# Kernel optimization log

Measured on AMD Instinct MI355X. Metric: run time of the kernel, lower is better.

## Reference

```python
import jax, jax.numpy as jnp
import numpy as np

KSIZE, STRIDE, RATE, FUSE_K, SCALE = 3, 1, 2, 3, 10.0
ESCAPE_NAN = 1e-4


def same_pad(x, k, s):
    # torch same_padding: pad so out = ceil(in/s)
    H, W = x.shape[2], x.shape[3]
    oh, ow = -(-H // s), -(-W // s)
    ph = max(0, (oh - 1) * s + k - H)
    pw = max(0, (ow - 1) * s + k - W)
    return jnp.pad(x, ((0, 0), (0, 0), (ph // 2, ph - ph // 2), (pw // 2, pw - pw // 2)))


def extract_patches(x, k, s):
    # torch Unfold -> view(B,C,k,k,L) -> permute(0,4,1,2,3): returns [B, L, C, k, k]
    x = same_pad(x, k, s)
    B, C, H, W = x.shape
    oh, ow = (H - k) // s + 1, (W - k) // s + 1
    rows = jnp.arange(oh)[:, None] * s + jnp.arange(k)[None, :]
    cols = jnp.arange(ow)[:, None] * s + jnp.arange(k)[None, :]
    p = x[:, :, rows][:, :, :, :, cols]  # [B,C,oh,k,ow,k]
    return p.transpose(0, 2, 4, 1, 3, 5).reshape(B, oh * ow, C, k, k)


def conv1x1(x, w, b):
    return jnp.einsum('bchw,oc->bohw', x, w) + b[None, :, None, None]


def conv2d(x, w):
    return jax.lax.conv_general_dilated(x, w, (1, 1), 'VALID',
                                        dimension_numbers=('NCHW', 'OIHW', 'NCHW'))


def conv_transpose2d(x, w, stride, pad):
    # matches F.conv_transpose2d(x, w[Cin,Cout,k,k], stride, padding=pad)
    k = w.shape[2]
    wf = jnp.flip(w, (2, 3))
    return jax.lax.conv_general_dilated(x, wf, (1, 1), [(k - 1 - pad, k - 1 - pad)] * 2,
                                        lhs_dilation=(stride, stride),
                                        dimension_numbers=('NCHW', 'IOHW', 'NCHW'))


def global_attention(a, bm, c, wq, bq, wk, bk, wv, bv, gamma):
    # a,bm: [B,C,H,W]; c: [B,1,Hc,Wc]; mask scales score rows before softmax
    B, C, H, W = a.shape
    dr = c.shape[2] // H
    c = c[:, :, ::dr, ::dr]  # nearest downsample, matches F.interpolate(mode='nearest')
    q = conv1x1(a, wq, bq).reshape(B, C, H * W)
    k = conv1x1(bm, wk, bk).reshape(B, C, H * W)
    sim = jnp.einsum('bci,bcj->bij', q, k)  # [B,N,N]
    mv = c.reshape(B, H * W)
    attn = jax.nn.softmax(sim * mv[:, :, None], axis=-1)
    v = conv1x1(a, wv, bv).reshape(B, C, H * W)
    out = jnp.einsum('bcj,bij->bci', v, attn).reshape(B, C, H, W)
    return gamma * a * c + (1.0 - c) * out


def _forward(f, b, mask, fa, pa):
    B, C, H, W = b.shape
    kernel = 2 * RATE
    raw_w = extract_patches(b, kernel, RATE * STRIDE)  # [B, L, C, 4, 4]
    f_ds = f[:, :, ::RATE, ::RATE]
    b_ds = b[:, :, ::RATE, ::RATE]
    Hd, Wd = f_ds.shape[2], f_ds.shape[3]
    mask0 = mask[0:1]  # torch uses m_groups[0] for all samples
    dr = mask0.shape[2] // Hd
    mask_ds = mask0[:, :, ::dr, ::dr]  # [1,1,Hd,Wd]
    w = extract_patches(b_ds, KSIZE, STRIDE)   # [B, L, C, 3, 3]
    fw = extract_patches(f_ds, KSIZE, STRIDE)  # [B, L, C, 3, 3]
    m = extract_patches(mask_ds, KSIZE, STRIDE)[0]  # [L, 1, 3, 3]
    mm = (jnp.mean(m, axis=(1, 2, 3), keepdims=True) == 0.0).astype(f.dtype)
    mm = mm.transpose(1, 0, 2, 3)  # [1, L, 1, 1]
    fuse_w = jnp.eye(FUSE_K, dtype=f.dtype).reshape(1, 1, FUSE_K, FUSE_K)

    def per_sample(xi, bi, fi_p, wi_p, raw_wi):
        # patch-level attention refines the dynamic conv kernels
        fp_p = global_attention(fi_p, wi_p, m, *pa)  # [L, C, 3, 3]
        norm = jnp.sqrt(jnp.sum(fp_p * fp_p, axis=(1, 2, 3), keepdims=True))
        wi_n = fp_p / jnp.maximum(norm, ESCAPE_NAN)
        # feature-level attention on the downsampled foreground
        fp = global_attention(xi[None], bi[None], mask_ds, *fa)  # [1,C,Hd,Wd]
        yi = conv2d(same_pad(fp, KSIZE, 1), wi_n)  # [1, L, Hd, Wd]
        Nb = Hd * Wd
        # fuse: identity-kernel smoothing over (bg-pos, fg-pos) score plane, twice
        yi = yi.reshape(1, 1, Nb, Nb)
        yi = conv2d(same_pad(yi, FUSE_K, 1), fuse_w)
        yi = yi.reshape(1, Hd, Wd, Hd, Wd).transpose(0, 2, 1, 4, 3).reshape(1, 1, Nb, Nb)
        yi = conv2d(same_pad(yi, FUSE_K, 1), fuse_w)
        yi = yi.reshape(1, Wd, Hd, Wd, Hd).transpose(0, 2, 1, 4, 3)
        yi = yi.reshape(1, Nb, Hd, Wd)
        yi = jax.nn.softmax(yi * mm * SCALE, axis=1) * mm
        return conv_transpose2d(yi, raw_wi, RATE, 1)[0] / 4.0  # [C, H, W]

    return jax.vmap(per_sample)(f_ds, b_ds, fw, w, raw_w)


def setup_inputs() -> dict:
    key = jax.random.key(0)
    ks = jax.random.split(key, 10)
    B, C, H, W = 2, 64, 96, 96
    f = jax.random.normal(ks[0], (B, C, H, W), jnp.float32)
    b = jax.random.normal(ks[1], (B, C, H, W), jnp.float32)
    mask = (jax.random.uniform(ks[2], (B, 1, H, W)) < 0.25).astype(jnp.float32)

    def wmat(k):
        return jax.random.normal(k, (C, C), jnp.float32) * 0.05

    return {
        'f': f, 'b': b, 'mask': mask,
        'fa_wq': wmat(ks[3]), 'fa_bq': jnp.zeros((C,), jnp.float32),
        'fa_wk': wmat(ks[4]), 'fa_bk': jnp.zeros((C,), jnp.float32),
        'fa_wv': wmat(ks[5]), 'fa_bv': jnp.zeros((C,), jnp.float32),
        'fa_gamma': jnp.ones((1,), jnp.float32),
        'pa_wq': wmat(ks[6]), 'pa_bq': jnp.zeros((C,), jnp.float32),
        'pa_wk': wmat(ks[7]), 'pa_bk': jnp.zeros((C,), jnp.float32),
        'pa_wv': wmat(ks[8]), 'pa_bv': jnp.zeros((C,), jnp.float32),
        'pa_gamma': jnp.ones((1,), jnp.float32),
    }


def reference(f, b, mask, fa_wq, fa_bq, fa_wk, fa_bk, fa_wv, fa_bv, fa_gamma,
              pa_wq, pa_bq, pa_wk, pa_bk, pa_wv, pa_bv, pa_gamma):
    fa = (fa_wq, fa_bq, fa_wk, fa_bk, fa_wv, fa_bv, fa_gamma)
    pa = (pa_wq, pa_bq, pa_wk, pa_bk, pa_wv, pa_bv, pa_gamma)
    return _forward(f, b, mask, fa, pa)
```

## Files before the change

### kernel.cpp

```cpp
#include <hip/hip_runtime.h>
#include <math.h>

#define HD 48
#define NB 2304
#define NC 64
#define IMG 96
#define NP 2401
#define KP 2432

#define CDIV(a,b) (((a)+(b)-1)/(b))

typedef unsigned short u16;
typedef __attribute__((ext_vector_type(8))) short  s16x8;
typedef __attribute__((ext_vector_type(8))) unsigned short u16x8;
typedef __attribute__((ext_vector_type(4))) float  f32x4;

constexpr size_t O_MASKDS = 0;
constexpr size_t O_MMP    = NB;
constexpr size_t O_CMAX   = (size_t)2*NB;
constexpr size_t O_CINV   = (size_t)4*NB;
constexpr size_t O_PMAX   = (size_t)6*NB;
constexpr size_t O_PSUM   = (size_t)38*NB;
constexpr size_t O_MEAN   = (size_t)70*NB;
constexpr size_t O_ACT    = (size_t)70*NB + 256;
constexpr size_t O_ROWIDX = O_ACT + 2434/1 + 62;
constexpr size_t O_INVROW = O_ROWIDX + 2560;
constexpr size_t O_NROW   = O_INVROW + NB;
constexpr size_t O_NEEDX  = O_NROW + 64;
constexpr size_t O_ZPAD   = O_NEEDX + NB;
constexpr size_t O_ARENA0 = O_NEEDX + NB + 64;
constexpr size_t A_FDS  = 0;
constexpr size_t A_FDST = 147456;
constexpr size_t A_SCR  = 294912;
constexpr size_t A_P0   = A_SCR + 2654208;
constexpr size_t A_P1   = A_P0 + (size_t)NB*NB;
constexpr size_t A_Y    = A_P1 + 5839232;
constexpr size_t A_B4   = A_Y + (size_t)NB*NB;
constexpr size_t SSTR   = A_B4 + 622592;
constexpr size_t TOTAL_F = O_ARENA0 + 2*SSTR;

__device__ inline void split_bf16(float x, u16& hi, u16& lo){
  unsigned int u = __float_as_uint(x);
  unsigned int r = u + 0x7FFFu + ((u >> 16) & 1u);
  hi = (u16)(r >> 16);
  float xh = __uint_as_float(((unsigned int)hi) << 16);
  float res = x - xh;
  unsigned int u2 = __float_as_uint(res);
  unsigned int r2 = u2 + 0x7FFFu + ((u2 >> 16) & 1u);
  lo = (u16)(r2 >> 16);
}

__device__ __forceinline__ void gload16(const u16* g, u16* l){
  __builtin_amdgcn_global_load_lds(
      (const __attribute__((address_space(1))) unsigned int*)g,
      (__attribute__((address_space(3))) unsigned int*)l, 16, 0, 0);
}


__global__ void k_prep(const float* __restrict__ mask, float* __restrict__ maskds,
                       float* __restrict__ mmP,
                       int* __restrict__ actIdx, int* __restrict__ nActPad,
                       int* __restrict__ rowIdx, int* __restrict__ invRow,
                       int* __restrict__ nRowPad, float* __restrict__ needXf,
                       u16* __restrict__ zp){
  __shared__ float lmm[NB];
  __shared__ unsigned char needX[NB], needS[NB];
  __shared__ int cnt[256], base[256];
  int tid = threadIdx.x;
  for(int q=tid; q<NB; q+=256){
    int hq = q/HD, wq = q%HD;
    maskds[q] = mask[(2*hq)*IMG + 2*wq];
    float any = 0.f;
    for(int u=-1;u<=1;u++)
      for(int v=-1;v<=1;v++){
        int y=hq+u, x=wq+v;
        if(y>=0&&y<HD&&x>=0&&x<HD) any += mask[(2*y)*IMG + 2*x];
      }
    float v = (any == 0.f) ? 1.f : 0.f;
    mmP[wq*HD + hq] = v;
    lmm[wq*HD + hq] = v;
  }
  if(tid < 16) ((unsigned int*)zp)[tid] = 0u;
  __syncthreads();
  {
    int c0 = tid*10, c1 = min(c0+10, NP);
    int flags = 0, lc = 0;
    for(int i=c0;i<c1;i++){
      int ph=i/49, pw=i%49;
      bool act=false;
      #pragma unroll
      for(int a=0;a<2;a++)
        #pragma unroll
        for(int bb=0;bb<2;bb++){
          int sh=ph-a, sw=pw-bb;
          if(sh>=0&&sh<HD&&sw>=0&&sw<HD && lmm[sw*HD+sh]!=0.f) act=true;
        }
      if(act){ flags |= 1<<(i-c0); lc++; }
    }
    cnt[tid]=lc;
    __syncthreads();
    if(tid==0){
      int run=0;
      for(int i=0;i<256;i++){ base[i]=run; run+=cnt[i]; }
      int pad=(run+63)&~63;
      nActPad[0]=pad; nActPad[1]=run;
      for(int k=run;k<pad;k++) actIdx[k]=NP;
    }
    __syncthreads();
    int o=base[tid];
    for(int i=c0;i<c1;i++) if(flags & (1<<(i-c0))) actIdx[o++]=i;
  }
  __syncthreads();
  {
    for(int i=tid;i<NB;i+=256) needX[i]=0;
    __syncthreads();
    for(int qp=tid; qp<NB; qp+=256){
      if(lmm[qp]!=0.f){
        #pragma unroll
        for(int d=-1;d<=1;d++){
          int rb=qp+d; if(rb<0||rb>=NB) continue;
          int b2=rb/HD, a=rb%HD;
          needX[a*HD + b2] = 1;
        }
      }
    }
    __syncthreads();
    for(int r=tid;r<NB;r+=256){
      unsigned char v = needX[r];
      if(r>0)    v |= needX[r-1];
      if(r<NB-1) v |= needX[r+1];
      needS[r]=v;
    }
    __syncthreads();
    int c0 = tid*9, c1 = min(c0+9, NB);
    int lc=0; for(int i=c0;i<c1;i++) lc += needS[i];
    cnt[tid]=lc;
    __syncthreads();
    if(tid==0){
      int run=0;
      for(int i=0;i<256;i++){ base[i]=run; run+=cnt[i]; }
      int pad=(run+127)&~127;
      nRowPad[0]=pad; nRowPad[1]=run;
      for(int k=run;k<pad;k++) rowIdx[k]=NB;
    }
    __syncthreads();
    int o=base[tid];
    for(int i=c0;i<c1;i++){
      if(needS[i]){ rowIdx[o]=i; invRow[i]=o; o++; }
      else invRow[i] = -1;
    }
    for(int i=tid;i<NB;i+=256) needXf[i] = needX[i] ? 1.f : 0.f;
  }
}

__global__ void k_ds(const float* __restrict__ src, float* __restrict__ fds0,
                     float* __restrict__ fdsT0){
  int s = blockIdx.y;
  float* fds  = fds0  + (size_t)s*SSTR;
  float* fdsT = fdsT0 + (size_t)s*SSTR;
  int idx = blockIdx.x*256 + threadIdx.x;
  if(idx >= NC*NB) return;
  int c = idx/NB, j = idx%NB;
  int h = j/HD, w = j%HD;
  float v = src[(((size_t)s*NC + c)*IMG + 2*h)*IMG + 2*w];
  fds[idx] = v;
  fdsT[(size_t)j*64 + c] = v;
}

__global__ void k_colmean(const float* __restrict__ fds0, float* __restrict__ meanf){
  int s = blockIdx.y;
  const float* fds = fds0 + (size_t)s*SSTR;
  int c = blockIdx.x;
  int tid = threadIdx.x;
  float sum = 0.f;
  for(int j=tid; j<NB; j+=256) sum += fds[(size_t)c*NB + j];
  for(int off=32; off>0; off>>=1) sum += __shfl_down(sum, off);
  __shared__ float red[4];
  if((tid&63)==0) red[tid>>6] = sum;
  __syncthreads();
  if(tid==0) meanf[s*64 + c] = (red[0]+red[1]+red[2]+red[3]) * (1.f/NB);
}

__global__ void k_meanvf(const float* __restrict__ meanf, const float* __restrict__ wv,
                         const float* __restrict__ bv, float* __restrict__ meanVf){
  int s = blockIdx.x;
  __shared__ float mf[64];
  int c = threadIdx.x;
  mf[c] = meanf[s*64 + c];
  __syncthreads();
  float sum = 0.f;
  for(int cc=0;cc<64;cc++) sum += wv[c*64+cc]*mf[cc];
  meanVf[s*64 + c] = sum + bv[c];
}

__global__ void k_stageA(const float* __restrict__ fdsT0, const float* __restrict__ maskds,
                         const float* __restrict__ wv, const float* __restrict__ bv,
                         const float* __restrict__ gammap,
                         u16* __restrict__ AH0, u16* __restrict__ AL0){
  int s = blockIdx.y;
  const float* fdsT = fdsT0 + (size_t)s*SSTR;
  u16* AH = AH0 + (size_t)s*2*SSTR;
  u16* AL = AL0 + (size_t)s*2*SSTR;
  __shared__ float sumA[4][64];
  __shared__ float mval[4][9];
  int wsl = threadIdx.x>>6;
  int c = threadIdx.x&63;
  int p = blockIdx.x*4 + wsl;
  int ph = p/HD, pw = p%HD;
  float A[9]; float sa = 0.f;
  #pragma unroll
  for(int i=0;i<9;i++){
    int u=i/3, v=i%3;
    int y=ph+u-1, x=pw+v-1;
    bool in = (y>=0&&y<HD&&x>=0&&x<HD);
    float fv = in ? fdsT[(size_t)(y*HD+x)*64 + c] : 0.f;
    A[i] = fv; sa += fv;
    if(c==0) mval[wsl][i] = in ? maskds[y*HD+x] : 0.f;
  }
  sumA[wsl][c] = sa;
  __syncthreads();
  float acc = 0.f;
  for(int cc=0;cc<64;cc++) acc += wv[c*64+cc]*sumA[wsl][cc];
  float meanVc = acc*(1.f/9.f) + bv[c];
  float gamma = gammap[0];
  float fpv[9]; float ss = 0.f;
  #pragma unroll
  for(int i=0;i<9;i++){
    float v = (mval[wsl][i]!=0.f) ? gamma*A[i] : meanVc;
    fpv[i] = v; ss += v*v;
  }
  for(int off=32; off>0; off>>=1) ss += __shfl_down(ss, off);
  ss = __shfl(ss, 0);
  float scale = 1.f / fmaxf(sqrtf(ss), 1e-4f);
  #pragma unroll
  for(int i=0;i<9;i++){
    u16 h,l; split_bf16(fpv[i]*scale, h, l);
    size_t o = (size_t)p*576 + c*9 + i;
    AH[o] = h; AL[o] = l;
  }
}

__global__ void k_bcolT_split(const float* __restrict__ fds0, const float* __restrict__ maskds,
                              const float* __restrict__ meanVf, const float* __restrict__ gfp,
                              u16* __restrict__ BTH0, u16* __restrict__ BTL0){
  int s = blockIdx.y;
  const float* fds = fds0 + (size_t)s*SSTR;
  u16* BTH = BTH0 + (size_t)s*2*SSTR;
  u16* BTL = BTL0 + (size_t)s*2*SSTR;
  int idx = blockIdx.x*256 + threadIdx.x;
  if(idx >= NB*576) return;
  int P = idx/576, k = idx%576;
  int c = k/9, i = k%9, u = i/3, v = i%3;
  int hP = P/HD, wP = P%HD;
  int y = hP+u-1, x = wP+v-1;
  float val = 0.f;
  if(y>=0&&y<HD&&x>=0&&x<HD){
    int pos = y*HD + x;
    val = (maskds[pos]!=0.f) ? gfp[0]*fds[(size_t)c*NB + pos] : meanVf[s*64 + c];
  }
  u16 h,l; split_bf16(val, h, l);
  BTH[idx] = h; BTL[idx] = l;
}

__global__ __launch_bounds__(256, 2)
void k_gemm4(const u16* __restrict__ AH0, const u16* __restrict__ AL0,
             const u16* __restrict__ BTH0, const u16* __restrict__ BTL0,
             float* __restrict__ C0, int M, int N, int Kparam, int nz,
             const int* __restrict__ Kdev,
             const int* __restrict__ rowIdx, const int* __restrict__ Mdev,
             const u16* __restrict__ zp,
             int ldA, int ldB, int ldC, long zstrC){
  __shared__ u16 sAH[2][128*32], sAL[2][128*32], sBH[2][128*32], sBL[2][128*32];
  int tid = threadIdx.x;
  int s = blockIdx.z / nz, zk = blockIdx.z % nz;
  int Mout = Mdev ? Mdev[0] : M;
  int gx = gridDim.x;
  int nwg = gx*gridDim.y;
  int orig = blockIdx.y*gx + blockIdx.x;
  int xcd = orig & 7;
  int qq = nwg>>3, rr2 = nwg&7;
  int swz = (xcd<rr2 ? xcd*(qq+1) : rr2*(qq+1) + (xcd-rr2)*qq) + (orig>>3);
  int by = swz/gx, bx = swz - by*gx;
  int m0 = by*128, n0 = bx*128;
  if(m0 >= Mout) return;
  const u16* AH  = AH0  + (size_t)s*2*SSTR;
  const u16* AL  = AL0  + (size_t)s*2*SSTR;
  const u16* BTH = BTH0 + (size_t)s*2*SSTR;
  const u16* BTL = BTL0 + (size_t)s*2*SSTR;
  float* Cz = C0 + (size_t)s*SSTR + (size_t)zk*zstrC;
  int K = Kdev ? Kdev[0] : Kparam;
  int Kc = (((K+31)/32 + nz - 1)/nz)*32;
  int kbeg = zk*Kc; int kend = kbeg+Kc; if(kend>K) kend=K;
  int w = tid>>6, lane = tid&63;
  int wr = w>>1, wc = w&1;
  int fr = lane&15, fq = lane>>4;

  int ch0 = w, ch1 = 4+w;
  int rl0 = ch0*16 + (lane>>2), rl1 = ch1*16 + (lane>>2);
  int gp = lane&3;
  int gr0 = (gp ^ ((rl0>>1)&3))*8;
  int gr1 = (gp ^ ((rl1>>1)&3))*8;
  int mi0 = m0+rl0, mi1 = m0+rl1;
  int ar0 = rowIdx ? rowIdx[mi0] : mi0;
  int ar1 = rowIdx ? rowIdx[mi1] : mi1;
  bool av0 = (ar0 < M), av1 = (ar1 < M);
  int br0 = n0+rl0, br1 = n0+rl1;
  bool bv0 = (br0 < N), bv1 = (br1 < N);
  const u16* pAH0 = AH + (size_t)(av0?ar0:0)*ldA + gr0;
  const u16* pAH1 = AH + (size_t)(av1?ar1:0)*ldA + gr1;
  const u16* pAL0 = AL + (size_t)(av0?ar0:0)*ldA + gr0;
  const u16* pAL1 = AL + (size_t)(av1?ar1:0)*ldA + gr1;
  const u16* pBH0 = BTH + (size_t)(bv0?br0:0)*ldB + gr0;
  const u16* pBH1 = BTH + (size_t)(bv1?br1:0)*ldB + gr1;
  const u16* pBL0 = BTL + (size_t)(bv0?br0:0)*ldB + gr0;
  const u16* pBL1 = BTL + (size_t)(bv1?br1:0)*ldB + gr1;
  int lo0 = ch0*512, lo1 = ch1*512;

#define GISSUE(BUF, K0) { \
    gload16(av0 ? pAH0+(K0) : zp, &sAH[BUF][lo0]); \
    gload16(av1 ? pAH1+(K0) : zp, &sAH[BUF][lo1]); \
    gload16(av0 ? pAL0+(K0) : zp, &sAL[BUF][lo0]); \
    gload16(av1 ? pAL1+(K0) : zp, &sAL[BUF][lo1]); \
    gload16(bv0 ? pBH0+(K0) : zp, &sBH[BUF][lo0]); \
    gload16(bv1 ? pBH1+(K0) : zp, &sBH[BUF][lo1]); \
    gload16(bv0 ? pBL0+(K0) : zp, &sBL[BUF][lo0]); \
    gload16(bv1 ? pBL1+(K0) : zp, &sBL[BUF][lo1]); }

  f32x4 acc[4][4];
  #pragma unroll
  for(int i=0;i<4;i++)
    #pragma unroll
    for(int j=0;j<4;j++) acc[i][j] = (f32x4){0.f,0.f,0.f,0.f};

  if(kbeg < kend){ GISSUE(0, kbeg); }
  __syncthreads();
  int cur = 0;
  for(int k0=kbeg; k0<kend; k0+=32){
    if(k0+32 < kend) GISSUE(cur^1, k0+32);
    s16x8 a_h[4],a_l[4],b_h[4],b_l[4];
    #pragma unroll
    for(int mi=0;mi<4;mi++){
      int row=wr*64+mi*16+fr; int gs=(fq^((row>>1)&3))*8;
      a_h[mi]=*(const s16x8*)&sAH[cur][row*32+gs];
      a_l[mi]=*(const s16x8*)&sAL[cur][row*32+gs];
    }
    #pragma unroll
    for(int ni=0;ni<4;ni++){
      int row=wc*64+ni*16+fr; int gs=(fq^((row>>1)&3))*8;
      b_h[ni]=*(const s16x8*)&sBH[cur][row*32+gs];
      b_l[ni]=*(const s16x8*)&sBL[cur][row*32+gs];
    }
    #pragma unroll
    for(int mi=0;mi<4;mi++)
      #pragma unroll
      for(int ni=0;ni<4;ni++){
        acc[mi][ni] = __builtin_amdgcn_mfma_f32_16x16x32_bf16(a_h[mi], b_h[ni], acc[mi][ni], 0,0,0);
        acc[mi][ni] = __builtin_amdgcn_mfma_f32_16x16x32_bf16(a_h[mi], b_l[ni], acc[mi][ni], 0,0,0);
        acc[mi][ni] = __builtin_amdgcn_mfma_f32_16x16x32_bf16(a_l[mi], b_h[ni], acc[mi][ni], 0,0,0);
      }
    __syncthreads();
    cur ^= 1;
  }
#undef GISSUE
  #pragma unroll
  for(int mi=0;mi<4;mi++)
    #pragma unroll
    for(int ni=0;ni<4;ni++){
      int row = m0 + wr*64 + mi*16 + fq*4;
      int col = n0 + wc*64 + ni*16 + fr;
      if(col < N){
        #pragma unroll
        for(int rr=0;rr<4;rr++)
          if(row+rr < Mout) Cz[(size_t)(row+rr)*ldC + col] = acc[mi][ni][rr];
      }
    }
}

__global__ void k_fuseP(const float* __restrict__ Sb, const int* __restrict__ invRow,
                        const float* __restrict__ needXf, float* __restrict__ Yb){
  int s = blockIdx.y;
  int r = blockIdx.x;
  if(needXf[r] == 0.f) return;
  const float* S = Sb + (size_t)s*SSTR;
  float* Y = Yb + (size_t)s*SSTR;
  int i0 = invRow[r];
  int im = (r>0)    ? invRow[r-1] : -1;
  int ip = (r<NB-1) ? invRow[r+1] : -1;
  __shared__ float lds[48*49];
  const float* row0 = S + (size_t)i0*NB;
  for(int t=threadIdx.x; t<NB; t+=256){
    float v = row0[t];
    if(im>=0 && t>0)    v += S[(size_t)im*NB + t-1];
    if(ip>=0 && t<NB-1) v += S[(size_t)ip*NB + t+1];
    lds[(t/HD)*49 + (t%HD)] = v;
  }
  __syncthreads();
  int a = r/HD, b2 = r%HD;
  float* orow = Y + (size_t)(b2*HD + a)*NB;
  for(int t=threadIdx.x; t<NB; t+=256){
    int d = t/HD, c = t%HD;
    orow[t] = lds[c*49 + d];
  }
}

__global__ void k_fuse_colsm(const float* __restrict__ Yb, const float* __restrict__ mmP,
                             float* __restrict__ pmax, float* __restrict__ psum){
  int s = blockIdx.z;
  const float* Y = Yb + (size_t)s*SSTR;
  int col = blockIdx.x*256 + threadIdx.x;
  int q0 = blockIdx.y*144;
  float mx = -1e30f, sum = 0.f;
  for(int q=q0; q<q0+144; q++){
    if(mmP[q] == 0.f) continue;
    float L = Y[(size_t)q*NB + col];
    if(q>0 && col>0)       L += Y[(size_t)(q-1)*NB + col-1];
    if(q<NB-1 && col<NB-1) L += Y[(size_t)(q+1)*NB + col+1];
    L *= 10.f;
    if(L > mx){ sum *= __expf(mx - L); mx = L; }
    sum += __expf(L - mx);
  }
  pmax[(size_t)(s*16 + blockIdx.y)*NB + col] = mx;
  psum[(size_t)(s*16 + blockIdx.y)*NB + col] = sum;
}

__global__ void k_combine(const float* __restrict__ pmax, const float* __restrict__ psum,
                          const float* __restrict__ mmP,
                          float* __restrict__ cmax, float* __restrict__ cinv){
  int s = blockIdx.y;
  int col = blockIdx.x*256 + threadIdx.x;
  int tid = threadIdx.x;
  __shared__ float redc[4];
  float cnt = 0.f;
  for(int k=tid; k<NB; k+=256) cnt += mmP[k];
  for(int off=32; off>0; off>>=1) cnt += __shfl_down(cnt, off);
  if((tid&63)==0) redc[tid>>6] = cnt;
  __syncthreads();
  float nAct = redc[0]+redc[1]+redc[2]+redc[3];
  float M = -1e30f;
  for(int k=0;k<16;k++) M = fmaxf(M, pmax[(size_t)(s*16+k)*NB + col]);
  if(nAct < NB - 0.5f) M = fmaxf(M, 0.f);
  float S = 0.f;
  for(int k=0;k<16;k++){
    float pm = pmax[(size_t)(s*16+k)*NB + col];
    float ps = psum[(size_t)(s*16+k)*NB + col];
    S += ps * __expf(pm - M);
  }
  S += ((float)NB - nAct) * __expf(0.f - M);
  cmax[s*NB + col] = M;
  cinv[s*NB + col] = 1.f/S;
}

__global__ void k_fuse_apply(const float* __restrict__ Yb, const float* __restrict__ mmP,
                             const float* __restrict__ cmax, const float* __restrict__ cinv,
                             float* __restrict__ yiTb){
  int s = blockIdx.y;
  const float* Y = Yb + (size_t)s*SSTR;
  float* yiT = yiTb + (size_t)s*SSTR;
  const float* cm = cmax + s*NB;
  const float* ci = cinv + s*NB;
  __shared__ float lds[48*49];
  int alpha = blockIdx.x/HD, delta = blockIdx.x%HD;
  for(int t=threadIdx.x; t<NB; t+=256){
    int beta = t/HD, gamma = t%HD;
    int qp = beta*HD + alpha;
    int Pp = delta*HD + gamma;
    float v = 0.f;
    if(mmP[qp] != 0.f){
      float L = Y[(size_t)qp*NB + Pp];
      if(qp>0 && Pp>0)       L += Y[(size_t)(qp-1)*NB + Pp-1];
      if(qp<NB-1 && Pp<NB-1) L += Y[(size_t)(qp+1)*NB + Pp+1];
      v = __expf(10.f*L - cm[Pp]) * ci[Pp];
    }
    lds[beta*49 + gamma] = v;
  }
  __syncthreads();
  for(int t=threadIdx.x; t<NB; t+=256){
    int gamma = t/HD, beta = t%HD;
    if(mmP[beta*HD + alpha] != 0.f)
      yiT[(size_t)(gamma*HD + delta)*NB + alpha*HD + beta] = lds[beta*49 + gamma];
  }
}

__global__ void k_zbuildT_split(const float* __restrict__ yiTb, const float* __restrict__ mmP,
                                const int* __restrict__ actIdx, const int* __restrict__ nActPad,
                                u16* __restrict__ UTH0, u16* __restrict__ UTL0){
  int s = blockIdx.z;
  const float* yiT = yiTb + (size_t)s*SSTR;
  u16* UTH = UTH0 + (size_t)s*2*SSTR;
  u16* UTL = UTL0 + (size_t)s*2*SSTR;
  int row = blockIdx.y;
  int cc  = blockIdx.x*256 + threadIdx.x;
  if(cc >= nActPad[0]) return;
  int pp = actIdx[cc];
  float z = 0.f;
  if(pp < NP){
    int rho = row/49, sig = row%49;
    int ph = pp/49, pw = pp%49;
    #pragma unroll
    for(int a=0;a<2;a++)
      #pragma unroll
      for(int bb=0;bb<2;bb++){
        int sh=ph-a, sw=pw-bb, rr=rho-a, ss=sig-bb;
        if(sh>=0 && sh<HD && sw>=0 && sw<HD && rr>=0 && rr<HD && ss>=0 && ss<HD
           && mmP[sw*HD+sh] != 0.f)
          z += yiT[(size_t)(rr*HD+ss)*NB + sh*HD+sw];
      }
  }
  u16 h,l; split_bf16(z, h, l);
  size_t o = (size_t)row*KP + cc;
  UTH[o] = h; UTL[o] = l;
}

__global__ void k_b4_split(const float* __restrict__ b,
                           const int* __restrict__ actIdx, const int* __restrict__ nActPad,
                           u16* __restrict__ B4H0, u16* __restrict__ B4L0){
  int s = blockIdx.y;
  u16* B4H = B4H0 + (size_t)s*2*SSTR;
  u16* B4L = B4L0 + (size_t)s*2*SSTR;
  int idx = blockIdx.x*256 + threadIdx.x;
  if(idx >= 256*KP) return;
  int m = idx/KP, kk = idx%KP;
  if(kk >= nActPad[0]) return;
  int pp = actIdx[kk];
  float val = 0.f;
  if(pp < NP){
    int phase = m>>6, c = m&63;
    int py = phase>>1, px = phase&1;
    int ph = pp/49, pw = pp%49;
    int y = 2*ph - py, x = 2*pw - px;
    if(y>=0&&y<IMG&&x>=0&&x<IMG) val = b[(((size_t)s*NC + c)*IMG + y)*IMG + x];
  }
  u16 h,l; split_bf16(val, h, l);
  B4H[idx] = h; B4L[idx] = l;
}

__global__ void k_epi(const float* __restrict__ Gb, float* __restrict__ out){
  int s = blockIdx.y;
  const float* G = Gb + (size_t)s*SSTR;
  int idx = blockIdx.x*256 + threadIdx.x;
  if(idx >= NC*IMG*IMG) return;
  int c = idx/(IMG*IMG), rem = idx%(IMG*IMG);
  int y = rem/IMG, x = rem%IMG;
  int py = y&1, px = x&1, r = y>>1, s2 = x>>1;
  size_t gi = (size_t)((py*2+px)*64 + c)*NP + (r+py)*49 + (s2+px);
  const size_t gz = (size_t)256*NP;
  float v = G[gi] + G[gi+gz] + G[gi+2*gz] + G[gi+3*gz];
  out[((size_t)s*NC + c)*IMG*IMG + rem] = v * 0.25f;
}

extern "C" void kernel_launch(void* const* d_in, const int* in_sizes, int n_in,
                              void* d_out, int out_size, void* d_ws, size_t ws_size,
                              hipStream_t stream){
  const float* f    = (const float*)d_in[0];
  const float* b    = (const float*)d_in[1];
  const float* mask = (const float*)d_in[2];
  const float* fa_wv=(const float*)d_in[7];  const float* fa_bv=(const float*)d_in[8];
  const float* fa_g =(const float*)d_in[9];
  const float* pa_wv=(const float*)d_in[14]; const float* pa_bv=(const float*)d_in[15];
  const float* pa_g =(const float*)d_in[16];
  float* out = (float*)d_out;
  float* ws  = (float*)d_ws;
  if(ws_size < TOTAL_F*sizeof(float)) return;

  float* maskds = ws + O_MASKDS;
  float* mmP    = ws + O_MMP;
  float* cmax   = ws + O_CMAX;
  float* cinv   = ws + O_CINV;
  float* pmax   = ws + O_PMAX;
  float* psum   = ws + O_PSUM;
  float* meanf  = ws + O_MEAN;
  float* meanVf = ws + O_MEAN + 128;
  int*   actIdx  = (int*)(ws + O_ACT);
  int*   nActPad = actIdx + 2432;
  int*   rowIdx  = (int*)(ws + O_ROWIDX);
  int*   invRow  = (int*)(ws + O_INVROW);
  int*   nRowPad = (int*)(ws + O_NROW);
  float* needXf  = ws + O_NEEDX;
  u16*   zp      = (u16*)(ws + O_ZPAD);

  float* fds0  = ws + O_ARENA0 + A_FDS;
  float* fdsT0 = ws + O_ARENA0 + A_FDST;
  u16*   AH0   = (u16*)(ws + O_ARENA0 + A_SCR);
  u16*   AL0   = AH0 + (size_t)NB*576;
  u16*   BTH0  = AL0 + (size_t)NB*576;
  u16*   BTL0  = BTH0 + (size_t)NB*576;
  float* G0    = ws + O_ARENA0 + A_SCR;
  float* Scmp0 = ws + O_ARENA0 + A_P0;
  float* Y0    = ws + O_ARENA0 + A_Y;
  float* yiT0  = Scmp0;
  u16*   UTH0  = (u16*)(ws + O_ARENA0 + A_P1);
  u16*   UTL0  = UTH0 + (size_t)NP*KP;
  u16*   B4H0  = (u16*)(ws + O_ARENA0 + A_B4);
  u16*   B4L0  = B4H0 + (size_t)256*KP;

  k_prep<<<1, 256, 0, stream>>>(mask, maskds, mmP, actIdx, nActPad,
                                rowIdx, invRow, nRowPad, needXf, zp);
  k_ds<<<dim3(CDIV(NC*NB,256), 2), 256, 0, stream>>>(f, fds0, fdsT0);
  k_colmean<<<dim3(64, 2), 256, 0, stream>>>(fds0, meanf);
  k_meanvf<<<2, 64, 0, stream>>>(meanf, fa_wv, fa_bv, meanVf);
  k_stageA<<<dim3(NB/4, 2), 256, 0, stream>>>(fdsT0, maskds, pa_wv, pa_bv, pa_g, AH0, AL0);
  k_bcolT_split<<<dim3(CDIV(NB*576,256), 2), 256, 0, stream>>>(fds0, maskds, meanVf, fa_g, BTH0, BTL0);

  k_gemm4<<<dim3(18,18,2), 256, 0, stream>>>(AH0, AL0, BTH0, BTL0, Scmp0,
      NB, NB, 576, 1, nullptr, rowIdx, nRowPad, zp, 576, 576, NB, 0L);

  k_fuseP<<<dim3(NB, 2), 256, 0, stream>>>(Scmp0, invRow, needXf, Y0);
  k_fuse_colsm<<<dim3(9,16,2), 256, 0, stream>>>(Y0, mmP, pmax, psum);
  k_combine<<<dim3(9, 2), 256, 0, stream>>>(pmax, psum, mmP, cmax, cinv);
  k_fuse_apply<<<dim3(NB, 2), 256, 0, stream>>>(Y0, mmP, cmax, cinv, yiT0);

  k_zbuildT_split<<<dim3(CDIV(KP,256), NP, 2), 256, 0, stream>>>(yiT0, mmP, actIdx, nActPad, UTH0, UTL0);
  k_b4_split<<<dim3(CDIV(256*KP,256), 2), 256, 0, stream>>>(b, actIdx, nActPad, B4H0, B4L0);
  k_gemm4<<<dim3(CDIV(NP,128), 2, 8), 256, 0, stream>>>(B4H0, B4L0, UTH0, UTL0, G0,
      256, NP, KP, 4, nActPad, nullptr, nullptr, zp, KP, KP, NP, (long)256*NP);
  k_epi<<<dim3(CDIV(NC*IMG*IMG,256), 2), 256, 0, stream>>>(G0, out);
}
```

Baseline: 224.9 us.

## Merge setup, stage-A/B, combine and operand-build kernels to cut launches

Folds prep, downsample and column-mean into one k_setup kernel, which drops the separate fds buffer. It also merges the A and B operand builds into one kernel, switching the K ordering to tap-major/channel-minor on both operands consistently. The column softmax combine step is recomputed inside k_fuse_apply for each block, using a mask count precomputed in setup. The Z-build and B4 split kernels are merged into a single grid. The aim is to remove several small launches and their dependencies, at the cost of redundant per-block combine work and branchier kernels.

```diff
diff --git a/kernel.cpp b/kernel.cpp
--- a/kernel.cpp
+++ b/kernel.cpp
@@ -17,8 +17,6 @@
 
 constexpr size_t O_MASKDS = 0;
 constexpr size_t O_MMP    = NB;
-constexpr size_t O_CMAX   = (size_t)2*NB;
-constexpr size_t O_CINV   = (size_t)4*NB;
 constexpr size_t O_PMAX   = (size_t)6*NB;
 constexpr size_t O_PSUM   = (size_t)38*NB;
 constexpr size_t O_MEAN   = (size_t)70*NB;
@@ -29,7 +27,6 @@
 constexpr size_t O_NEEDX  = O_NROW + 64;
 constexpr size_t O_ZPAD   = O_NEEDX + NB;
 constexpr size_t O_ARENA0 = O_NEEDX + NB + 64;
-constexpr size_t A_FDS  = 0;
 constexpr size_t A_FDST = 147456;
 constexpr size_t A_SCR  = 294912;
 constexpr size_t A_P0   = A_SCR + 2654208;
@@ -57,16 +54,43 @@
 }
 
 
-__global__ void k_prep(const float* __restrict__ mask, float* __restrict__ maskds,
-                       float* __restrict__ mmP,
-                       int* __restrict__ actIdx, int* __restrict__ nActPad,
-                       int* __restrict__ rowIdx, int* __restrict__ invRow,
-                       int* __restrict__ nRowPad, float* __restrict__ needXf,
-                       u16* __restrict__ zp){
+__global__ void k_setup(const float* __restrict__ f, const float* __restrict__ mask,
+                        float* __restrict__ fdsT0, float* __restrict__ meanf,
+                        float* __restrict__ maskds, float* __restrict__ mmP,
+                        int* __restrict__ actIdx, int* __restrict__ nActPad,
+                        int* __restrict__ rowIdx, int* __restrict__ invRow,
+                        int* __restrict__ nRowPad, float* __restrict__ needXf,
+                        u16* __restrict__ zp, float* __restrict__ nActQ){
   __shared__ float lmm[NB];
   __shared__ unsigned char needX[NB], needS[NB];
   __shared__ int cnt[256], base[256];
+  int s = blockIdx.y;
+  int bx = blockIdx.x;
   int tid = threadIdx.x;
+  if(bx < 576){
+    float* fdsT = fdsT0 + (size_t)s*SSTR;
+    int idx = bx*256 + tid;
+    int c = idx/NB, j = idx%NB;
+    int h = j/HD, w = j%HD;
+    float v = f[(((size_t)s*NC + c)*IMG + 2*h)*IMG + 2*w];
+    fdsT[(size_t)j*64 + c] = v;
+    return;
+  }
+  if(bx < 640){
+    int c = bx - 576;
+    float sum = 0.f;
+    for(int j=tid; j<NB; j+=256){
+      int h = j/HD, w = j%HD;
+      sum += f[(((size_t)s*NC + c)*IMG + 2*h)*IMG + 2*w];
+    }
+    for(int off=32; off>0; off>>=1) sum += __shfl_down(sum, off);
+    __shared__ float red[4];
+    if((tid&63)==0) red[tid>>6] = sum;
+    __syncthreads();
+    if(tid==0) meanf[s*64 + c] = (red[0]+red[1]+red[2]+red[3]) * (1.f/NB);
+    return;
+  }
+  if(s != 0) return;
   for(int q=tid; q<NB; q+=256){
     int hq = q/HD, wq = q%HD;
     maskds[q] = mask[(2*hq)*IMG + 2*wq];
@@ -81,6 +105,17 @@
     lmm[wq*HD + hq] = v;
   }
   if(tid < 16) ((unsigned int*)zp)[tid] = 0u;
+  __syncthreads();
+  {
+    float cnta = 0.f;
+    for(int q=tid; q<NB; q+=256) cnta += lmm[q];
+    for(int off=32; off>0; off>>=1) cnta += __shfl_down(cnta, off);
+    if((tid&63)==0) ((volatile float*)needXf)[0] = 0.f;
+    __shared__ float redc[4];
+    if((tid&63)==0) redc[tid>>6] = cnta;
+    __syncthreads();
+    if(tid==0) nActQ[0] = redc[0]+redc[1]+redc[2]+redc[3];
+  }
   __syncthreads();
   {
     int c0 = tid*10, c1 = min(c0+10, NP);
@@ -153,34 +188,6 @@
   }
 }
 
-__global__ void k_ds(const float* __restrict__ src, float* __restrict__ fds0,
-                     float* __restrict__ fdsT0){
-  int s = blockIdx.y;
-  float* fds  = fds0  + (size_t)s*SSTR;
-  float* fdsT = fdsT0 + (size_t)s*SSTR;
-  int idx = blockIdx.x*256 + threadIdx.x;
-  if(idx >= NC*NB) return;
-  int c = idx/NB, j = idx%NB;
-  int h = j/HD, w = j%HD;
-  float v = src[(((size_t)s*NC + c)*IMG + 2*h)*IMG + 2*w];
-  fds[idx] = v;
-  fdsT[(size_t)j*64 + c] = v;
-}
-
-__global__ void k_colmean(const float* __restrict__ fds0, float* __restrict__ meanf){
-  int s = blockIdx.y;
-  const float* fds = fds0 + (size_t)s*SSTR;
-  int c = blockIdx.x;
-  int tid = threadIdx.x;
-  float sum = 0.f;
-  for(int j=tid; j<NB; j+=256) sum += fds[(size_t)c*NB + j];
-  for(int off=32; off>0; off>>=1) sum += __shfl_down(sum, off);
-  __shared__ float red[4];
-  if((tid&63)==0) red[tid>>6] = sum;
-  __syncthreads();
-  if(tid==0) meanf[s*64 + c] = (red[0]+red[1]+red[2]+red[3]) * (1.f/NB);
-}
-
 __global__ void k_meanvf(const float* __restrict__ meanf, const float* __restrict__ wv,
                          const float* __restrict__ bv, float* __restrict__ meanVf){
   int s = blockIdx.x;
@@ -193,73 +200,73 @@
   meanVf[s*64 + c] = sum + bv[c];
 }
 
-__global__ void k_stageA(const float* __restrict__ fdsT0, const float* __restrict__ maskds,
-                         const float* __restrict__ wv, const float* __restrict__ bv,
-                         const float* __restrict__ gammap,
-                         u16* __restrict__ AH0, u16* __restrict__ AL0){
+__global__ void k_stageAB(const float* __restrict__ fdsT0, const float* __restrict__ maskds,
+                          const float* __restrict__ pwv, const float* __restrict__ pbv,
+                          const float* __restrict__ pg,
+                          const float* __restrict__ meanVf, const float* __restrict__ gfp,
+                          u16* __restrict__ AH0, u16* __restrict__ AL0,
+                          u16* __restrict__ BTH0, u16* __restrict__ BTL0){
   int s = blockIdx.y;
   const float* fdsT = fdsT0 + (size_t)s*SSTR;
-  u16* AH = AH0 + (size_t)s*2*SSTR;
-  u16* AL = AL0 + (size_t)s*2*SSTR;
-  __shared__ float sumA[4][64];
-  __shared__ float mval[4][9];
-  int wsl = threadIdx.x>>6;
-  int c = threadIdx.x&63;
-  int p = blockIdx.x*4 + wsl;
-  int ph = p/HD, pw = p%HD;
-  float A[9]; float sa = 0.f;
-  #pragma unroll
-  for(int i=0;i<9;i++){
-    int u=i/3, v=i%3;
-    int y=ph+u-1, x=pw+v-1;
-    bool in = (y>=0&&y<HD&&x>=0&&x<HD);
-    float fv = in ? fdsT[(size_t)(y*HD+x)*64 + c] : 0.f;
-    A[i] = fv; sa += fv;
-    if(c==0) mval[wsl][i] = in ? maskds[y*HD+x] : 0.f;
-  }
-  sumA[wsl][c] = sa;
-  __syncthreads();
-  float acc = 0.f;
-  for(int cc=0;cc<64;cc++) acc += wv[c*64+cc]*sumA[wsl][cc];
-  float meanVc = acc*(1.f/9.f) + bv[c];
-  float gamma = gammap[0];
-  float fpv[9]; float ss = 0.f;
-  #pragma unroll
-  for(int i=0;i<9;i++){
-    float v = (mval[wsl][i]!=0.f) ? gamma*A[i] : meanVc;
-    fpv[i] = v; ss += v*v;
-  }
-  for(int off=32; off>0; off>>=1) ss += __shfl_down(ss, off);
-  ss = __shfl(ss, 0);
-  float scale = 1.f / fmaxf(sqrtf(ss), 1e-4f);
-  #pragma unroll
-  for(int i=0;i<9;i++){
-    u16 h,l; split_bf16(fpv[i]*scale, h, l);
-    size_t o = (size_t)p*576 + c*9 + i;
-    AH[o] = h; AL[o] = l;
-  }
-}
-
-__global__ void k_bcolT_split(const float* __restrict__ fds0, const float* __restrict__ maskds,
-                              const float* __restrict__ meanVf, const float* __restrict__ gfp,
-                              u16* __restrict__ BTH0, u16* __restrict__ BTL0){
-  int s = blockIdx.y;
-  const float* fds = fds0 + (size_t)s*SSTR;
-  u16* BTH = BTH0 + (size_t)s*2*SSTR;
-  u16* BTL = BTL0 + (size_t)s*2*SSTR;
-  int idx = blockIdx.x*256 + threadIdx.x;
-  if(idx >= NB*576) return;
-  int P = idx/576, k = idx%576;
-  int c = k/9, i = k%9, u = i/3, v = i%3;
-  int hP = P/HD, wP = P%HD;
-  int y = hP+u-1, x = wP+v-1;
-  float val = 0.f;
-  if(y>=0&&y<HD&&x>=0&&x<HD){
-    int pos = y*HD + x;
-    val = (maskds[pos]!=0.f) ? gfp[0]*fds[(size_t)c*NB + pos] : meanVf[s*64 + c];
-  }
-  u16 h,l; split_bf16(val, h, l);
-  BTH[idx] = h; BTL[idx] = l;
+  int bx = blockIdx.x;
+  if(bx < 576){
+    u16* AH = AH0 + (size_t)s*2*SSTR;
+    u16* AL = AL0 + (size_t)s*2*SSTR;
+    __shared__ float sumA[4][64];
+    __shared__ float mval[4][9];
+    int wsl = threadIdx.x>>6;
+    int c = threadIdx.x&63;
+    int p = bx*4 + wsl;
+    int ph = p/HD, pw = p%HD;
+    float A[9]; float sa = 0.f;
+    #pragma unroll
+    for(int i=0;i<9;i++){
+      int u=i/3, v=i%3;
+      int y=ph+u-1, x=pw+v-1;
+      bool in = (y>=0&&y<HD&&x>=0&&x<HD);
+      float fv = in ? fdsT[(size_t)(y*HD+x)*64 + c] : 0.f;
+      A[i] = fv; sa += fv;
+      if(c==0) mval[wsl][i] = in ? maskds[y*HD+x] : 0.f;
+    }
+    sumA[wsl][c] = sa;
+    __syncthreads();
+    float acc = 0.f;
+    for(int cc=0;cc<64;cc++) acc += pwv[c*64+cc]*sumA[wsl][cc];
+    float meanVc = acc*(1.f/9.f) + pbv[c];
+    float gamma = pg[0];
+    float fpv[9]; float ss = 0.f;
+    #pragma unroll
+    for(int i=0;i<9;i++){
+      float v = (mval[wsl][i]!=0.f) ? gamma*A[i] : meanVc;
+      fpv[i] = v; ss += v*v;
+    }
+    for(int off=32; off>0; off>>=1) ss += __shfl_down(ss, off);
+    ss = __shfl(ss, 0);
+    float scale = 1.f / fmaxf(sqrtf(ss), 1e-4f);
+    #pragma unroll
+    for(int i=0;i<9;i++){
+      u16 h,l; split_bf16(fpv[i]*scale, h, l);
+      size_t o = (size_t)p*576 + i*64 + c;
+      AH[o] = h; AL[o] = l;
+    }
+  } else {
+    u16* BTH = BTH0 + (size_t)s*2*SSTR;
+    u16* BTL = BTL0 + (size_t)s*2*SSTR;
+    int idx = (bx-576)*256 + threadIdx.x;
+    if(idx >= NB*576) return;
+    int P = idx/576, k = idx%576;
+    int i = k>>6, c = k&63;
+    int u = i/3, v = i%3;
+    int hP = P/HD, wP = P%HD;
+    int y = hP+u-1, x = wP+v-1;
+    float val = 0.f;
+    if(y>=0&&y<HD&&x>=0&&x<HD){
+      int pos = y*HD + x;
+      val = (maskds[pos]!=0.f) ? gfp[0]*fdsT[(size_t)pos*64 + c] : meanVf[s*64 + c];
+    }
+    u16 h,l; split_bf16(val, h, l);
+    BTH[idx] = h; BTL[idx] = l;
+  }
 }
 
 __global__ __launch_bounds__(256, 2)
@@ -423,43 +430,29 @@
   psum[(size_t)(s*16 + blockIdx.y)*NB + col] = sum;
 }
 
-__global__ void k_combine(const float* __restrict__ pmax, const float* __restrict__ psum,
-                          const float* __restrict__ mmP,
-                          float* __restrict__ cmax, float* __restrict__ cinv){
-  int s = blockIdx.y;
-  int col = blockIdx.x*256 + threadIdx.x;
-  int tid = threadIdx.x;
-  __shared__ float redc[4];
-  float cnt = 0.f;
-  for(int k=tid; k<NB; k+=256) cnt += mmP[k];
-  for(int off=32; off>0; off>>=1) cnt += __shfl_down(cnt, off);
-  if((tid&63)==0) redc[tid>>6] = cnt;
-  __syncthreads();
-  float nAct = redc[0]+redc[1]+redc[2]+redc[3];
-  float M = -1e30f;
-  for(int k=0;k<16;k++) M = fmaxf(M, pmax[(size_t)(s*16+k)*NB + col]);
-  if(nAct < NB - 0.5f) M = fmaxf(M, 0.f);
-  float S = 0.f;
-  for(int k=0;k<16;k++){
-    float pm = pmax[(size_t)(s*16+k)*NB + col];
-    float ps = psum[(size_t)(s*16+k)*NB + col];
-    S += ps * __expf(pm - M);
-  }
-  S += ((float)NB - nAct) * __expf(0.f - M);
-  cmax[s*NB + col] = M;
-  cinv[s*NB + col] = 1.f/S;
-}
-
 __global__ void k_fuse_apply(const float* __restrict__ Yb, const float* __restrict__ mmP,
-                             const float* __restrict__ cmax, const float* __restrict__ cinv,
+                             const float* __restrict__ pmax, const float* __restrict__ psum,
+                             const float* __restrict__ nActQ,
                              float* __restrict__ yiTb){
   int s = blockIdx.y;
   const float* Y = Yb + (size_t)s*SSTR;
   float* yiT = yiTb + (size_t)s*SSTR;
-  const float* cm = cmax + s*NB;
-  const float* ci = cinv + s*NB;
   __shared__ float lds[48*49];
+  __shared__ float lcm[48], lci[48];
   int alpha = blockIdx.x/HD, delta = blockIdx.x%HD;
+  float nAct = nActQ[0];
+  for(int t=threadIdx.x; t<48; t+=256){
+    int Pp = delta*HD + t;
+    float M = -1e30f;
+    for(int k=0;k<16;k++) M = fmaxf(M, pmax[(size_t)(s*16+k)*NB + Pp]);
+    if(nAct < NB - 0.5f) M = fmaxf(M, 0.f);
+    float S = 0.f;
+    for(int k=0;k<16;k++)
+      S += psum[(size_t)(s*16+k)*NB + Pp] * __expf(pmax[(size_t)(s*16+k)*NB + Pp] - M);
+    S += ((float)NB - nAct) * __expf(0.f - M);
+    lcm[t] = M; lci[t] = 1.f/S;
+  }
+  __syncthreads();
   for(int t=threadIdx.x; t<NB; t+=256){
     int beta = t/HD, gamma = t%HD;
     int qp = beta*HD + alpha;
@@ -469,7 +462,7 @@
       float L = Y[(size_t)qp*NB + Pp];
       if(qp>0 && Pp>0)       L += Y[(size_t)(qp-1)*NB + Pp-1];
       if(qp<NB-1 && Pp<NB-1) L += Y[(size_t)(qp+1)*NB + Pp+1];
-      v = __expf(10.f*L - cm[Pp]) * ci[Pp];
+      v = __expf(10.f*L - lcm[gamma]) * lci[gamma];
     }
     lds[beta*49 + gamma] = v;
   }
@@ -481,57 +474,57 @@
   }
 }
 
-__global__ void k_zbuildT_split(const float* __restrict__ yiTb, const float* __restrict__ mmP,
-                                const int* __restrict__ actIdx, const int* __restrict__ nActPad,
-                                u16* __restrict__ UTH0, u16* __restrict__ UTL0){
+__global__ void k_zb4(const float* __restrict__ yiTb, const float* __restrict__ mmP,
+                      const int* __restrict__ actIdx, const int* __restrict__ nActPad,
+                      const float* __restrict__ b,
+                      u16* __restrict__ UTH0, u16* __restrict__ UTL0,
+                      u16* __restrict__ B4H0, u16* __restrict__ B4L0){
   int s = blockIdx.z;
-  const float* yiT = yiTb + (size_t)s*SSTR;
-  u16* UTH = UTH0 + (size_t)s*2*SSTR;
-  u16* UTL = UTL0 + (size_t)s*2*SSTR;
-  int row = blockIdx.y;
-  int cc  = blockIdx.x*256 + threadIdx.x;
-  if(cc >= nActPad[0]) return;
-  int pp = actIdx[cc];
-  float z = 0.f;
-  if(pp < NP){
-    int rho = row/49, sig = row%49;
-    int ph = pp/49, pw = pp%49;
-    #pragma unroll
-    for(int a=0;a<2;a++)
+  if(blockIdx.y < NP){
+    const float* yiT = yiTb + (size_t)s*SSTR;
+    u16* UTH = UTH0 + (size_t)s*2*SSTR;
+    u16* UTL = UTL0 + (size_t)s*2*SSTR;
+    int row = blockIdx.y;
+    int cc  = blockIdx.x*256 + threadIdx.x;
+    if(cc >= nActPad[0]) return;
+    int pp = actIdx[cc];
+    float z = 0.f;
+    if(pp < NP){
+      int rho = row/49, sig = row%49;
+      int ph = pp/49, pw = pp%49;
       #pragma unroll
-      for(int bb=0;bb<2;bb++){
-        int sh=ph-a, sw=pw-bb, rr=rho-a, ss=sig-bb;
-        if(sh>=0 && sh<HD && sw>=0 && sw<HD && rr>=0 && rr<HD && ss>=0 && ss<HD
-           && mmP[sw*HD+sh] != 0.f)
-          z += yiT[(size_t)(rr*HD+ss)*NB + sh*HD+sw];
-      }
-  }
-  u16 h,l; split_bf16(z, h, l);
-  size_t o = (size_t)row*KP + cc;
-  UTH[o] = h; UTL[o] = l;
-}
-
-__global__ void k_b4_split(const float* __restrict__ b,
-                           const int* __restrict__ actIdx, const int* __restrict__ nActPad,
-                           u16* __restrict__ B4H0, u16* __restrict__ B4L0){
-  int s = blockIdx.y;
-  u16* B4H = B4H0 + (size_t)s*2*SSTR;
-  u16* B4L = B4L0 + (size_t)s*2*SSTR;
-  int idx = blockIdx.x*256 + threadIdx.x;
-  if(idx >= 256*KP) return;
-  int m = idx/KP, kk = idx%KP;
-  if(kk >= nActPad[0]) return;
-  int pp = actIdx[kk];
-  float val = 0.f;
-  if(pp < NP){
-    int phase = m>>6, c = m&63;
-    int py = phase>>1, px = phase&1;
-    int ph = pp/49, pw = pp%49;
-    int y = 2*ph - py, x = 2*pw - px;
-    if(y>=0&&y<IMG&&x>=0&&x<IMG) val = b[(((size_t)s*NC + c)*IMG + y)*IMG + x];
-  }
-  u16 h,l; split_bf16(val, h, l);
-  B4H[idx] = h; B4L[idx] = l;
+      for(int a=0;a<2;a++)
+        #pragma unroll
+        for(int bb=0;bb<2;bb++){
+          int sh=ph-a, sw=pw-bb, rr=rho-a, ss=sig-bb;
+          if(sh>=0 && sh<HD && sw>=0 && sw<HD && rr>=0 && rr<HD && ss>=0 && ss<HD
+             && mmP[sw*HD+sh] != 0.f)
+            z += yiT[(size_t)(rr*HD+ss)*NB + sh*HD+sw];
+        }
+    }
+    u16 h,l; split_bf16(z, h, l);
+    size_t o = (size_t)row*KP + cc;
+    UTH[o] = h; UTL[o] = l;
+  } else {
+    u16* B4H = B4H0 + (size_t)s*2*SSTR;
+    u16* B4L = B4L0 + (size_t)s*2*SSTR;
+    int j = (blockIdx.y - NP)*10 + blockIdx.x;
+    int idx = j*256 + threadIdx.x;
+    if(idx >= 256*KP) return;
+    int m = idx/KP, kk = idx%KP;
+    if(kk >= nActPad[0]) return;
+    int pp = actIdx[kk];
+    float val = 0.f;
+    if(pp < NP){
+      int phase = m>>6, c = m&63;
+      int py = phase>>1, px = phase&1;
+      int ph = pp/49, pw = pp%49;
+      int y = 2*ph - py, x = 2*pw - px;
+      if(y>=0&&y<IMG&&x>=0&&x<IMG) val = b[(((size_t)s*NC + c)*IMG + y)*IMG + x];
+    }
+    u16 h,l; split_bf16(val, h, l);
+    B4H[idx] = h; B4L[idx] = l;
+  }
 }
 
 __global__ void k_epi(const float* __restrict__ Gb, float* __restrict__ out){
@@ -564,8 +557,6 @@
 
   float* maskds = ws + O_MASKDS;
   float* mmP    = ws + O_MMP;
-  float* cmax   = ws + O_CMAX;
-  float* cinv   = ws + O_CINV;
   float* pmax   = ws + O_PMAX;
   float* psum   = ws + O_PSUM;
   float* meanf  = ws + O_MEAN;
@@ -577,8 +568,8 @@
   int*   nRowPad = (int*)(ws + O_NROW);
   float* needXf  = ws + O_NEEDX;
   u16*   zp      = (u16*)(ws + O_ZPAD);
-
-  float* fds0  = ws + O_ARENA0 + A_FDS;
+  float* nActQ   = ws + O_ZPAD + 32;
+
   float* fdsT0 = ws + O_ARENA0 + A_FDST;
   u16*   AH0   = (u16*)(ws + O_ARENA0 + A_SCR);
   u16*   AL0   = AH0 + (size_t)NB*576;
@@ -593,24 +584,21 @@
   u16*   B4H0  = (u16*)(ws + O_ARENA0 + A_B4);
   u16*   B4L0  = B4H0 + (size_t)256*KP;
 
-  k_prep<<<1, 256, 0, stream>>>(mask, maskds, mmP, actIdx, nActPad,
-                                rowIdx, invRow, nRowPad, needXf, zp);
-  k_ds<<<dim3(CDIV(NC*NB,256), 2), 256, 0, stream>>>(f, fds0, fdsT0);
-  k_colmean<<<dim3(64, 2), 256, 0, stream>>>(fds0, meanf);
+  k_setup<<<dim3(641, 2), 256, 0, stream>>>(f, mask, fdsT0, meanf, maskds, mmP,
+      actIdx, nActPad, rowIdx, invRow, nRowPad, needXf, zp, nActQ);
   k_meanvf<<<2, 64, 0, stream>>>(meanf, fa_wv, fa_bv, meanVf);
-  k_stageA<<<dim3(NB/4, 2), 256, 0, stream>>>(fdsT0, maskds, pa_wv, pa_bv, pa_g, AH0, AL0);
-  k_bcolT_split<<<dim3(CDIV(NB*576,256), 2), 256, 0, stream>>>(fds0, maskds, meanVf, fa_g, BTH0, BTL0);
+  k_stageAB<<<dim3(576+5184, 2), 256, 0, stream>>>(fdsT0, maskds,
+      pa_wv, pa_bv, pa_g, meanVf, fa_g, AH0, AL0, BTH0, BTL0);
 
   k_gemm4<<<dim3(18,18,2), 256, 0, stream>>>(AH0, AL0, BTH0, BTL0, Scmp0,
       NB, NB, 576, 1, nullptr, rowIdx, nRowPad, zp, 576, 576, NB, 0L);
 
   k_fuseP<<<dim3(NB, 2), 256, 0, stream>>>(Scmp0, invRow, needXf, Y0);
   k_fuse_colsm<<<dim3(9,16,2), 256, 0, stream>>>(Y0, mmP, pmax, psum);
-  k_combine<<<dim3(9, 2), 256, 0, stream>>>(pmax, psum, mmP, cmax, cinv);
-  k_fuse_apply<<<dim3(NB, 2), 256, 0, stream>>>(Y0, mmP, cmax, cinv, yiT0);
-
-  k_zbuildT_split<<<dim3(CDIV(KP,256), NP, 2), 256, 0, stream>>>(yiT0, mmP, actIdx, nActPad, UTH0, UTL0);
-  k_b4_split<<<dim3(CDIV(256*KP,256), 2), 256, 0, stream>>>(b, actIdx, nActPad, B4H0, B4L0);
+  k_fuse_apply<<<dim3(NB, 2), 256, 0, stream>>>(Y0, mmP, pmax, psum, nActQ, yiT0);
+
+  k_zb4<<<dim3(10, NP+244, 2), 256, 0, stream>>>(yiT0, mmP, actIdx, nActPad, b,
+      UTH0, UTL0, B4H0, B4L0);
   k_gemm4<<<dim3(CDIV(NP,128), 2, 8), 256, 0, stream>>>(B4H0, B4L0, UTH0, UTL0, G0,
       256, NP, KP, 4, nActPad, nullptr, nullptr, zp, KP, KP, NP, (long)256*NP);
   k_epi<<<dim3(CDIV(NC*IMG*IMG,256), 2), 256, 0, stream>>>(G0, out);
```

Result: faster. 216.5 us (-3.8%).
